# Kernel tuning notes

Hardware: AMD Instinct MI355X
Metric: run time of the kernel (lower is better)

## Reference

```python
import jax, jax.numpy as jnp
import numpy as np

N_NODES = 50000
N_EDGES = 800000


def setup_inputs() -> dict:
    key = jax.random.key(0)
    ks = jax.random.split(key, 8)
    return {
        "x": jax.random.normal(ks[0], (N_NODES, 256), dtype=jnp.float32),
        "adj_vals": jax.random.uniform(ks[1], (N_EDGES,), dtype=jnp.float32),
        "rows": jax.random.randint(ks[2], (N_EDGES,), 0, N_NODES, dtype=jnp.int32),
        "cols": jax.random.randint(ks[3], (N_EDGES,), 0, N_NODES, dtype=jnp.int32),
        "W1": jax.random.normal(ks[4], (256, 256), dtype=jnp.float32) * (1.0 / np.sqrt(256)),
        "b1": jnp.zeros((256,), dtype=jnp.float32),
        "W2": jax.random.normal(ks[5], (256, 256), dtype=jnp.float32) * (1.0 / np.sqrt(256)),
        "b2": jnp.zeros((256,), dtype=jnp.float32),
        "W3": jax.random.normal(ks[6], (256, 128), dtype=jnp.float32) * (1.0 / np.sqrt(256)),
        "b3": jnp.zeros((128,), dtype=jnp.float32),
    }


def reference(x, adj_vals, rows, cols, W1, b1, W2, b2, W3, b3):
    n = x.shape[0]

    def spmm(h):
        # sparse adjacency matmul: out[r] += val * h[c] over all edges (r, c)
        return jax.ops.segment_sum(adj_vals[:, None] * h[cols], rows, num_segments=n)

    # GCNLayer: adj @ (x @ W) + b ; ReLU between layers (dropout p=0 => identity)
    h = jax.nn.relu(spmm(x @ W1) + b1)
    h = jax.nn.relu(spmm(h @ W2) + b2)
    return spmm(h @ W3) + b3
```

## Files before the change

### kernel.cpp

```cpp
#include <hip/hip_runtime.h>
#include <hip/hip_bf16.h>


#define N_NODES 50000
#define N_EDGES 800000
#define KDIM 256
#define BK 32
#define ELLCAP 64
#define ELLB 782
#define TRB 640

typedef __attribute__((ext_vector_type(8))) short short8;
typedef __attribute__((ext_vector_type(4))) float f32x4;

__device__ __forceinline__ ushort f2bf(float f) {
    union { float f; unsigned u; } x; x.f = f;
    unsigned r = x.u + 0x7fffu + ((x.u >> 16) & 1u);
    return (ushort)(r >> 16);
}
__device__ __forceinline__ float bf2f(ushort u) {
    union { unsigned u; float f; } x; x.u = ((unsigned)u) << 16;
    return x.f;
}

__device__ __forceinline__ void gld_lds16(const void* g, void* l) {
    __builtin_amdgcn_global_load_lds(
        (const __attribute__((address_space(1))) void*)g,
        (__attribute__((address_space(3))) void*)l, 16, 0, 0);
}

__global__ __launch_bounds__(256) void transpose_ell_kernel(
        const float* __restrict__ W1, const float* __restrict__ W2,
        const float* __restrict__ W3, ushort* __restrict__ Wt1,
        ushort* __restrict__ Wt2, ushort* __restrict__ Wt3,
        const int* __restrict__ rows, const int* __restrict__ cols,
        const float* __restrict__ vals, int* __restrict__ cnt,
        int2* __restrict__ cv) {
    int b = blockIdx.x;
    if (b < TRB) {
        int id = b * 256 + threadIdx.x;
        if (id < 65536) {
            int n = id >> 8, k = id & 255;
            Wt1[n * 256 + k] = f2bf(W1[k * 256 + n]);
        } else if (id < 131072) {
            int i = id - 65536, n = i >> 8, k = i & 255;
            Wt2[n * 256 + k] = f2bf(W2[k * 256 + n]);
        } else {
            int i = id - 131072, n = i >> 8, k = i & 255;
            Wt3[n * 256 + k] = f2bf(W3[k * 128 + n]);
        }
    } else {
        int e0 = ((b - TRB) * 256 + threadIdx.x) * 4;
        if (e0 < N_EDGES) {
            int4   r4 = *(const int4*)&rows[e0];
            int4   c4 = *(const int4*)&cols[e0];
            float4 v4 = *(const float4*)&vals[e0];
            int p0 = atomicAdd(&cnt[r4.x], 1);
            cv[(r4.x << 6) + p0] = make_int2(c4.x, __float_as_int(v4.x));
            int p1 = atomicAdd(&cnt[r4.y], 1);
            cv[(r4.y << 6) + p1] = make_int2(c4.y, __float_as_int(v4.y));
            int p2 = atomicAdd(&cnt[r4.z], 1);
            cv[(r4.z << 6) + p2] = make_int2(c4.z, __float_as_int(v4.z));
            int p3 = atomicAdd(&cnt[r4.w], 1);
            cv[(r4.w << 6) + p3] = make_int2(c4.w, __float_as_int(v4.w));
        }
    }
}


template <bool AFP32>
__device__ __forceinline__ void gemm_body(
        const void* __restrict__ Ain, const ushort* __restrict__ Wt,
        ushort* __restrict__ C, int M, int N, int bx, int by) {
    __shared__ char smem[AFP32 ? 49152 : 32768];
    const int ABYTES = AFP32 ? 16384 : 8192;

    int t = threadIdx.x;
    int lane = t & 63;
    int w = t >> 6;
    int wbase = w * 64;
    int row0 = bx * 128, col0 = by * 128;
    int wm2 = w & 1, wn2 = w >> 1;
    int wm = wm2 * 64, wn = wn2 * 64;
    int q = lane >> 4, mi = lane & 15;

    char* Ab0 = smem;
    char* Ab1 = smem + ABYTES;
    char* Bb0 = smem + 2 * ABYTES;
    char* Bb1 = smem + 2 * ABYTES + 8192;

    const float*  Af = (const float*)Ain;
    const ushort* Au = (const ushort*)Ain;

    auto stageA = [&](char* dst, int k0) {
        if (AFP32) {
            #pragma unroll
            for (int i = 0; i < 4; i++) {
                int D = i * 256 + t;
                int h = D >> 9, s = D & 511;
                int f = s >> 6, lp = s & 63;
                int row = row0 + (f >> 2) * 64 + (f & 3) * 16 + (lp & 15);
                if (row >= M) row = M - 1;
                const float* g = Af + (size_t)row * KDIM + k0 + (lp >> 4) * 8 + h * 4;
                gld_lds16(g, dst + (i * 256 + wbase) * 16);
            }
        } else {
            #pragma unroll
            for (int i = 0; i < 2; i++) {
                int D = i * 256 + t;
                int f = D >> 6, lp = D & 63;
                int row = row0 + (f >> 2) * 64 + (f & 3) * 16 + (lp & 15);
                if (row >= M) row = M - 1;
                const ushort* g = Au + (size_t)row * KDIM + k0 + (lp >> 4) * 8;
                gld_lds16(g, dst + (i * 256 + wbase) * 16);
            }
        }
    };
    auto stageB = [&](char* dst, int k0) {
        #pragma unroll
        for (int i = 0; i < 2; i++) {
            int D = i * 256 + t;
            int f = D >> 6, lp = D & 63;
            int col = col0 + (f >> 2) * 64 + (f & 3) * 16 + (lp & 15);
            const ushort* g = Wt + (size_t)col * KDIM + k0 + (lp >> 4) * 8;
            gld_lds16(g, dst + (i * 256 + wbase) * 16);
        }
    };

    f32x4 acc[4][4];
    #pragma unroll
    for (int i = 0; i < 4; i++)
        #pragma unroll
        for (int j = 0; j < 4; j++) acc[i][j] = (f32x4)0.f;

    stageA(Ab0, 0);
    stageB(Bb0, 0);
    __syncthreads();

    #pragma unroll
    for (int kt = 0; kt < 8; kt++) {
        char* Acur = (kt & 1) ? Ab1 : Ab0;
        char* Bcur = (kt & 1) ? Bb1 : Bb0;
        if (kt < 7) {
            stageA((kt & 1) ? Ab0 : Ab1, (kt + 1) * BK);
            stageB((kt & 1) ? Bb0 : Bb1, (kt + 1) * BK);
        }

        short8 af[4], bfr[4];
        if (AFP32) {
            const float* As = (const float*)Acur;
            #pragma unroll
            for (int mt = 0; mt < 4; mt++) {
                int gA = (wm2 * 4 + mt) * 64 + lane;
                f32x4 lo = *(const f32x4*)(As + gA * 4);
                f32x4 hi = *(const f32x4*)(As + 2048 + gA * 4);
                af[mt][0] = (short)f2bf(lo[0]); af[mt][1] = (short)f2bf(lo[1]);
                af[mt][2] = (short)f2bf(lo[2]); af[mt][3] = (short)f2bf(lo[3]);
                af[mt][4] = (short)f2bf(hi[0]); af[mt][5] = (short)f2bf(hi[1]);
                af[mt][6] = (short)f2bf(hi[2]); af[mt][7] = (short)f2bf(hi[3]);
            }
        } else {
            #pragma unroll
            for (int mt = 0; mt < 4; mt++)
                af[mt] = *(const short8*)(Acur + ((wm2 * 4 + mt) * 64 + lane) * 16);
        }
        #pragma unroll
        for (int nt = 0; nt < 4; nt++)
            bfr[nt] = *(const short8*)(Bcur + ((wn2 * 4 + nt) * 64 + lane) * 16);

        #pragma unroll
        for (int mt = 0; mt < 4; mt++)
            #pragma unroll
            for (int nt = 0; nt < 4; nt++)
                acc[mt][nt] = __builtin_amdgcn_mfma_f32_16x16x32_bf16(
                    af[mt], bfr[nt], acc[mt][nt], 0, 0, 0);

        __syncthreads();
    }

    ushort* Cs = (ushort*)smem;
    #pragma unroll
    for (int mt = 0; mt < 4; mt++)
        #pragma unroll
        for (int r = 0; r < 4; r++)
            #pragma unroll
            for (int nt = 0; nt < 4; nt++)
                Cs[(wm + mt * 16 + q * 4 + r) * 128 + wn + nt * 16 + mi] =
                    f2bf(acc[mt][nt][r]);
    __syncthreads();
    #pragma unroll
    for (int i = 0; i < 8; i++) {
        int idx = i * 256 + t;
        int rr = idx >> 4, gc = idx & 15;
        int grow = row0 + rr;
        if (grow < M)
            *(short8*)&C[(size_t)grow * N + col0 + gc * 8] =
                *(const short8*)&Cs[rr * 128 + gc * 8];
    }
}

template <bool AFP32>
__global__ __launch_bounds__(256) void gemm_bf16_kernel(
        const void* __restrict__ Ain, const ushort* __restrict__ Wt,
        ushort* __restrict__ C, int M, int N) {
    gemm_body<AFP32>(Ain, Wt, C, M, N, blockIdx.x, blockIdx.y);
}


template <int F, bool RELU, bool OUT_BF16>
__global__ __launch_bounds__(256) void spmm_kernel(
        const ushort* __restrict__ H, const int* __restrict__ cnt,
        const int2* __restrict__ cv, const float* __restrict__ bias,
        void* __restrict__ out, int nrows) {
    constexpr int FL = F / 8;
    constexpr int EP = 64 / FL;
    constexpr int STEP = EP * 8;
    int wave = threadIdx.x >> 6, lane = threadIdx.x & 63;
    int r = blockIdx.x * 4 + wave;
    if (r >= nrows) return;
    int fl = lane % FL, ep = lane / FL;
    const ushort* Hl = H + fl * 8;

    float acc[8];
    #pragma unroll
    for (int j = 0; j < 8; j++) acc[j] = 0.f;

    int start = r << 6;
    int end = start + cnt[r];
    for (int base = start; base < end; base += STEP) {
        int e0 = base + ep * 8;
        int4 ma = *(const int4*)&cv[e0];
        int4 mb = *(const int4*)&cv[e0 + 2];
        int4 mc = *(const int4*)&cv[e0 + 4];
        int4 md = *(const int4*)&cv[e0 + 6];
        int   c[8];
        float v[8];
        c[0] = ma.x; v[0] = __int_as_float(ma.y);
        c[1] = ma.z; v[1] = __int_as_float(ma.w);
        c[2] = mb.x; v[2] = __int_as_float(mb.y);
        c[3] = mb.z; v[3] = __int_as_float(mb.w);
        c[4] = mc.x; v[4] = __int_as_float(mc.y);
        c[5] = mc.z; v[5] = __int_as_float(mc.w);
        c[6] = md.x; v[6] = __int_as_float(md.y);
        c[7] = md.z; v[7] = __int_as_float(md.w);
        #pragma unroll
        for (int u = 0; u < 8; u++) {
            if (e0 + u >= end) { c[u] = 0; v[u] = 0.f; }
        }
        short8 h[8];
        #pragma unroll
        for (int u = 0; u < 8; u++)
            h[u] = *(const short8*)&Hl[(size_t)c[u] * F];
        #pragma unroll
        for (int j = 0; j < 8; j++) {
            #pragma unroll
            for (int u = 0; u < 8; u++)
                acc[j] += v[u] * bf2f((ushort)h[u][j]);
        }
    }

    #pragma unroll
    for (int off = FL; off < 64; off <<= 1)
        #pragma unroll
        for (int j = 0; j < 8; j++) acc[j] += __shfl_down(acc[j], off, 64);

    if (ep == 0) {
        #pragma unroll
        for (int j = 0; j < 8; j++) {
            float o = acc[j] + bias[fl * 8 + j];
            if (RELU) o = fmaxf(o, 0.f);
            acc[j] = o;
        }
        if (OUT_BF16) {
            short8 ob;
            #pragma unroll
            for (int j = 0; j < 8; j++) ob[j] = (short)f2bf(acc[j]);
            *(short8*)((ushort*)out + (size_t)r * F + fl * 8) = ob;
        } else {
            float* of = (float*)out + (size_t)r * F + fl * 8;
            *(float4*)&of[0] = make_float4(acc[0], acc[1], acc[2], acc[3]);
            *(float4*)&of[4] = make_float4(acc[4], acc[5], acc[6], acc[7]);
        }
    }
}


extern "C" void kernel_launch(void* const* d_in, const int* in_sizes, int n_in,
                              void* d_out, int out_size, void* d_ws, size_t ws_size,
                              hipStream_t stream) {
    const float* x    = (const float*)d_in[0];
    const float* av   = (const float*)d_in[1];
    const int*   rows = (const int*)d_in[2];
    const int*   cols = (const int*)d_in[3];
    const float* W1   = (const float*)d_in[4];
    const float* b1   = (const float*)d_in[5];
    const float* W2   = (const float*)d_in[6];
    const float* b2   = (const float*)d_in[7];
    const float* W3   = (const float*)d_in[8];
    const float* b3   = (const float*)d_in[9];
    float* out = (float*)d_out;

    const int N = N_NODES;

    char* p = (char*)d_ws;
    auto carve = [&](size_t bytes) {
        void* q = (void*)p;
        p += (bytes + 255) & ~(size_t)255;
        return q;
    };
    ushort* bufG = (ushort*)carve((size_t)N * 256 * 2);
    ushort* bufH = (ushort*)carve((size_t)N * 256 * 2);
    ushort* Wt1  = (ushort*)carve((size_t)256 * 256 * 2);
    ushort* Wt2  = (ushort*)carve((size_t)256 * 256 * 2);
    ushort* Wt3  = (ushort*)carve((size_t)128 * 256 * 2);
    int*    cnt  = (int*)carve((size_t)N * 4);
    int2*   cv   = (int2*)carve(((size_t)N * ELLCAP + 128) * 8);

    hipMemsetAsync(cnt, 0, (size_t)N * 4, stream);

    transpose_ell_kernel<<<TRB + ELLB, 256, 0, stream>>>(
        W1, W2, W3, Wt1, Wt2, Wt3, rows, cols, av, cnt, cv);

    gemm_bf16_kernel<true><<<dim3(391, 2), 256, 0, stream>>>(x, Wt1, bufG, N, 256);

    int spmm_blocks = (N + 3) / 4;
    spmm_kernel<256, true, true><<<spmm_blocks, 256, 0, stream>>>(bufG, cnt, cv, b1, bufH, N);
    gemm_bf16_kernel<false><<<dim3(391, 2), 256, 0, stream>>>(bufH, Wt2, bufG, N, 256);
    spmm_kernel<256, true, true><<<spmm_blocks, 256, 0, stream>>>(bufG, cnt, cv, b2, bufH, N);
    gemm_bf16_kernel<false><<<dim3(391, 1), 256, 0, stream>>>(bufH, Wt3, bufG, N, 128);
    spmm_kernel<128, false, false><<<spmm_blocks, 256, 0, stream>>>(bufG, cnt, cv, b3, out, N);
}
```

Measured before the change: 362.2 us.

## Pack ELL entries to 32 bits, pre-convert x to bf16, use full-width row GEMM

Each ELL entry now packs a 16-bit column index and an fp16 value into 32 bits, halving edge metadata traffic in the three SpMM passes. A new prep kernel converts x from fp32 to bf16 up front, so the first GEMM reads bf16. The GEMM is restructured so each block owns 64 rows across the full output width, loading each A tile once. Packing the column index into 16 bits only holds because node ids stay below 65536, and fp16 edge values lose precision.

Result: no change. 360.2 us (-0.6%).

```diff
diff --git a/kernel.cpp b/kernel.cpp
--- a/kernel.cpp
+++ b/kernel.cpp
@@ -1,5 +1,5 @@
 #include <hip/hip_runtime.h>
-#include <hip/hip_bf16.h>
+#include <hip/hip_fp16.h>
 
 
 #define N_NODES 50000
@@ -7,7 +7,8 @@
 #define KDIM 256
 #define BK 32
 #define ELLCAP 64
-#define ELLB 782
+#define ELLB 391
+#define XCB 3125
 #define TRB 640
 
 typedef __attribute__((ext_vector_type(8))) short short8;
@@ -29,16 +30,54 @@
         (__attribute__((address_space(3))) void*)l, 16, 0, 0);
 }
 
-__global__ __launch_bounds__(256) void transpose_ell_kernel(
+__global__ __launch_bounds__(256) void prep_kernel(
         const float* __restrict__ W1, const float* __restrict__ W2,
         const float* __restrict__ W3, ushort* __restrict__ Wt1,
         ushort* __restrict__ Wt2, ushort* __restrict__ Wt3,
         const int* __restrict__ rows, const int* __restrict__ cols,
         const float* __restrict__ vals, int* __restrict__ cnt,
-        int2* __restrict__ cv) {
+        unsigned* __restrict__ cvp, const float* __restrict__ x,
+        ushort* __restrict__ bufX) {
     int b = blockIdx.x;
-    if (b < TRB) {
-        int id = b * 256 + threadIdx.x;
+    if (b < ELLB) {
+        int e0 = (b * 256 + threadIdx.x) * 8;
+        if (e0 < N_EDGES) {
+            int4 ra = *(const int4*)&rows[e0];
+            int4 rb = *(const int4*)&rows[e0 + 4];
+            int4 ca = *(const int4*)&cols[e0];
+            int4 cb = *(const int4*)&cols[e0 + 4];
+            float4 va = *(const float4*)&vals[e0];
+            float4 vb = *(const float4*)&vals[e0 + 4];
+            int   r[8] = {ra.x, ra.y, ra.z, ra.w, rb.x, rb.y, rb.z, rb.w};
+            int   c[8] = {ca.x, ca.y, ca.z, ca.w, cb.x, cb.y, cb.z, cb.w};
+            float v[8] = {va.x, va.y, va.z, va.w, vb.x, vb.y, vb.z, vb.w};
+            #pragma unroll
+            for (int u = 0; u < 8; u++) {
+                int p = atomicAdd(&cnt[r[u]], 1);
+                unsigned pk = ((unsigned)c[u] << 16) |
+                              (unsigned)__half_as_ushort(__float2half_rn(v[u]));
+                cvp[(r[u] << 6) + p] = pk;
+            }
+        }
+    } else if (b < ELLB + XCB) {
+        int base = ((b - ELLB) * 256 + threadIdx.x) * 16;
+        float4 f0 = *(const float4*)&x[base];
+        float4 f1 = *(const float4*)&x[base + 4];
+        float4 f2 = *(const float4*)&x[base + 8];
+        float4 f3 = *(const float4*)&x[base + 12];
+        short8 o0, o1;
+        o0[0] = (short)f2bf(f0.x); o0[1] = (short)f2bf(f0.y);
+        o0[2] = (short)f2bf(f0.z); o0[3] = (short)f2bf(f0.w);
+        o0[4] = (short)f2bf(f1.x); o0[5] = (short)f2bf(f1.y);
+        o0[6] = (short)f2bf(f1.z); o0[7] = (short)f2bf(f1.w);
+        o1[0] = (short)f2bf(f2.x); o1[1] = (short)f2bf(f2.y);
+        o1[2] = (short)f2bf(f2.z); o1[3] = (short)f2bf(f2.w);
+        o1[4] = (short)f2bf(f3.x); o1[5] = (short)f2bf(f3.y);
+        o1[6] = (short)f2bf(f3.z); o1[7] = (short)f2bf(f3.w);
+        *(short8*)&bufX[base] = o0;
+        *(short8*)&bufX[base + 8] = o1;
+    } else {
+        int id = (b - ELLB - XCB) * 256 + threadIdx.x;
         if (id < 65536) {
             int n = id >> 8, k = id & 255;
             Wt1[n * 256 + k] = f2bf(W1[k * 256 + n]);
@@ -49,81 +88,42 @@
             int i = id - 131072, n = i >> 8, k = i & 255;
             Wt3[n * 256 + k] = f2bf(W3[k * 128 + n]);
         }
-    } else {
-        int e0 = ((b - TRB) * 256 + threadIdx.x) * 4;
-        if (e0 < N_EDGES) {
-            int4   r4 = *(const int4*)&rows[e0];
-            int4   c4 = *(const int4*)&cols[e0];
-            float4 v4 = *(const float4*)&vals[e0];
-            int p0 = atomicAdd(&cnt[r4.x], 1);
-            cv[(r4.x << 6) + p0] = make_int2(c4.x, __float_as_int(v4.x));
-            int p1 = atomicAdd(&cnt[r4.y], 1);
-            cv[(r4.y << 6) + p1] = make_int2(c4.y, __float_as_int(v4.y));
-            int p2 = atomicAdd(&cnt[r4.z], 1);
-            cv[(r4.z << 6) + p2] = make_int2(c4.z, __float_as_int(v4.z));
-            int p3 = atomicAdd(&cnt[r4.w], 1);
-            cv[(r4.w << 6) + p3] = make_int2(c4.w, __float_as_int(v4.w));
-        }
-    }
-}
-
-
-template <bool AFP32>
-__device__ __forceinline__ void gemm_body(
-        const void* __restrict__ Ain, const ushort* __restrict__ Wt,
-        ushort* __restrict__ C, int M, int N, int bx, int by) {
-    __shared__ char smem[AFP32 ? 49152 : 32768];
-    const int ABYTES = AFP32 ? 16384 : 8192;
+    }
+}
+
+
+template <int N>
+__global__ __launch_bounds__(N, 4) void gemm_rows_kernel(
+        const ushort* __restrict__ A, const ushort* __restrict__ Wt,
+        ushort* __restrict__ C, int M) {
+    __shared__ char smem[8192 + 2 * N * 64];
 
     int t = threadIdx.x;
     int lane = t & 63;
     int w = t >> 6;
-    int wbase = w * 64;
-    int row0 = bx * 128, col0 = by * 128;
-    int wm2 = w & 1, wn2 = w >> 1;
-    int wm = wm2 * 64, wn = wn2 * 64;
+    int row0 = blockIdx.x * 64;
+    int wn = w * 64;
     int q = lane >> 4, mi = lane & 15;
 
-    char* Ab0 = smem;
-    char* Ab1 = smem + ABYTES;
-    char* Bb0 = smem + 2 * ABYTES;
-    char* Bb1 = smem + 2 * ABYTES + 8192;
-
-    const float*  Af = (const float*)Ain;
-    const ushort* Au = (const ushort*)Ain;
-
-    auto stageA = [&](char* dst, int k0) {
-        if (AFP32) {
-            #pragma unroll
-            for (int i = 0; i < 4; i++) {
-                int D = i * 256 + t;
-                int h = D >> 9, s = D & 511;
-                int f = s >> 6, lp = s & 63;
-                int row = row0 + (f >> 2) * 64 + (f & 3) * 16 + (lp & 15);
-                if (row >= M) row = M - 1;
-                const float* g = Af + (size_t)row * KDIM + k0 + (lp >> 4) * 8 + h * 4;
-                gld_lds16(g, dst + (i * 256 + wbase) * 16);
-            }
-        } else {
-            #pragma unroll
-            for (int i = 0; i < 2; i++) {
-                int D = i * 256 + t;
-                int f = D >> 6, lp = D & 63;
-                int row = row0 + (f >> 2) * 64 + (f & 3) * 16 + (lp & 15);
-                if (row >= M) row = M - 1;
-                const ushort* g = Au + (size_t)row * KDIM + k0 + (lp >> 4) * 8;
-                gld_lds16(g, dst + (i * 256 + wbase) * 16);
-            }
+    auto stageA = [&](int bi, int k0) {
+        char* dst = smem + bi * 4096;
+        #pragma unroll
+        for (int i = 0; i < 256 / N; i++) {
+            int g = i * N + t;
+            int row = row0 + ((g >> 6) << 4) + (g & 15);
+            if (row >= M) row = M - 1;
+            const ushort* src = A + (size_t)row * KDIM + k0 + (((g & 63) >> 4) << 3);
+            gld_lds16(src, dst + (i * N + w * 64) * 16);
         }
     };
-    auto stageB = [&](char* dst, int k0) {
-        #pragma unroll
-        for (int i = 0; i < 2; i++) {
-            int D = i * 256 + t;
-            int f = D >> 6, lp = D & 63;
-            int col = col0 + (f >> 2) * 64 + (f & 3) * 16 + (lp & 15);
-            const ushort* g = Wt + (size_t)col * KDIM + k0 + (lp >> 4) * 8;
-            gld_lds16(g, dst + (i * 256 + wbase) * 16);
+    auto stageB = [&](int bi, int k0) {
+        char* dst = smem + 8192 + bi * (N * 64);
+        #pragma unroll
+        for (int i = 0; i < 4; i++) {
+            int g = i * N + t;
+            int col = ((g >> 6) << 4) + (g & 15);
+            const ushort* src = Wt + (size_t)col * KDIM + k0 + (((g & 63) >> 4) << 3);
+            gld_lds16(src, dst + (i * N + w * 64) * 16);
         }
     };
 
@@ -133,40 +133,27 @@
         #pragma unroll
         for (int j = 0; j < 4; j++) acc[i][j] = (f32x4)0.f;
 
-    stageA(Ab0, 0);
-    stageB(Bb0, 0);
+    stageA(0, 0);
+    stageB(0, 0);
     __syncthreads();
 
     #pragma unroll
     for (int kt = 0; kt < 8; kt++) {
-        char* Acur = (kt & 1) ? Ab1 : Ab0;
-        char* Bcur = (kt & 1) ? Bb1 : Bb0;
+        int cur = kt & 1;
         if (kt < 7) {
-            stageA((kt & 1) ? Ab0 : Ab1, (kt + 1) * BK);
-            stageB((kt & 1) ? Bb0 : Bb1, (kt + 1) * BK);
-        }
+            stageA(cur ^ 1, (kt + 1) * BK);
+            stageB(cur ^ 1, (kt + 1) * BK);
+        }
+        char* Ac = smem + cur * 4096;
+        char* Bc = smem + 8192 + cur * (N * 64);
 
         short8 af[4], bfr[4];
-        if (AFP32) {
-            const float* As = (const float*)Acur;
-            #pragma unroll
-            for (int mt = 0; mt < 4; mt++) {
-                int gA = (wm2 * 4 + mt) * 64 + lane;
-                f32x4 lo = *(const f32x4*)(As + gA * 4);
-                f32x4 hi = *(const f32x4*)(As + 2048 + gA * 4);
-                af[mt][0] = (short)f2bf(lo[0]); af[mt][1] = (short)f2bf(lo[1]);
-                af[mt][2] = (short)f2bf(lo[2]); af[mt][3] = (short)f2bf(lo[3]);
-                af[mt][4] = (short)f2bf(hi[0]); af[mt][5] = (short)f2bf(hi[1]);
-                af[mt][6] = (short)f2bf(hi[2]); af[mt][7] = (short)f2bf(hi[3]);
-            }
-        } else {
-            #pragma unroll
-            for (int mt = 0; mt < 4; mt++)
-                af[mt] = *(const short8*)(Acur + ((wm2 * 4 + mt) * 64 + lane) * 16);
-        }
+        #pragma unroll
+        for (int mt = 0; mt < 4; mt++)
+            af[mt] = *(const short8*)(Ac + (mt * 64 + lane) * 16);
         #pragma unroll
         for (int nt = 0; nt < 4; nt++)
-            bfr[nt] = *(const short8*)(Bcur + ((wn2 * 4 + nt) * 64 + lane) * 16);
+            bfr[nt] = *(const short8*)(Bc + ((w * 4 + nt) * 64 + lane) * 16);
 
         #pragma unroll
         for (int mt = 0; mt < 4; mt++)
@@ -185,32 +172,26 @@
         for (int r = 0; r < 4; r++)
             #pragma unroll
             for (int nt = 0; nt < 4; nt++)
-                Cs[(wm + mt * 16 + q * 4 + r) * 128 + wn + nt * 16 + mi] =
+                Cs[(mt * 16 + q * 4 + r) * N + wn + nt * 16 + mi] =
                     f2bf(acc[mt][nt][r]);
     __syncthreads();
+    constexpr int C8 = N / 8;
     #pragma unroll
     for (int i = 0; i < 8; i++) {
-        int idx = i * 256 + t;
-        int rr = idx >> 4, gc = idx & 15;
+        int idx = i * N + t;
+        int rr = idx / C8, gc = idx % C8;
         int grow = row0 + rr;
         if (grow < M)
-            *(short8*)&C[(size_t)grow * N + col0 + gc * 8] =
-                *(const short8*)&Cs[rr * 128 + gc * 8];
-    }
-}
-
-template <bool AFP32>
-__global__ __launch_bounds__(256) void gemm_bf16_kernel(
-        const void* __restrict__ Ain, const ushort* __restrict__ Wt,
-        ushort* __restrict__ C, int M, int N) {
-    gemm_body<AFP32>(Ain, Wt, C, M, N, blockIdx.x, blockIdx.y);
+            *(short8*)&C[(size_t)grow * N + gc * 8] =
+                *(const short8*)&Cs[rr * N + gc * 8];
+    }
 }
 
 
 template <int F, bool RELU, bool OUT_BF16>
 __global__ __launch_bounds__(256) void spmm_kernel(
         const ushort* __restrict__ H, const int* __restrict__ cnt,
-        const int2* __restrict__ cv, const float* __restrict__ bias,
+        const unsigned* __restrict__ cvp, const float* __restrict__ bias,
         void* __restrict__ out, int nrows) {
     constexpr int FL = F / 8;
     constexpr int EP = 64 / FL;
@@ -229,23 +210,16 @@
     int end = start + cnt[r];
     for (int base = start; base < end; base += STEP) {
         int e0 = base + ep * 8;
-        int4 ma = *(const int4*)&cv[e0];
-        int4 mb = *(const int4*)&cv[e0 + 2];
-        int4 mc = *(const int4*)&cv[e0 + 4];
-        int4 md = *(const int4*)&cv[e0 + 6];
+        uint4 ma = *(const uint4*)&cvp[e0];
+        uint4 mb = *(const uint4*)&cvp[e0 + 4];
+        unsigned mw[8] = {ma.x, ma.y, ma.z, ma.w, mb.x, mb.y, mb.z, mb.w};
         int   c[8];
         float v[8];
-        c[0] = ma.x; v[0] = __int_as_float(ma.y);
-        c[1] = ma.z; v[1] = __int_as_float(ma.w);
-        c[2] = mb.x; v[2] = __int_as_float(mb.y);
-        c[3] = mb.z; v[3] = __int_as_float(mb.w);
-        c[4] = mc.x; v[4] = __int_as_float(mc.y);
-        c[5] = mc.z; v[5] = __int_as_float(mc.w);
-        c[6] = md.x; v[6] = __int_as_float(md.y);
-        c[7] = md.z; v[7] = __int_as_float(md.w);
         #pragma unroll
         for (int u = 0; u < 8; u++) {
-            if (e0 + u >= end) { c[u] = 0; v[u] = 0.f; }
+            bool ok = (e0 + u < end);
+            c[u] = ok ? (int)(mw[u] >> 16) : 0;
+            v[u] = ok ? __half2float(__ushort_as_half((ushort)mw[u])) : 0.f;
         }
         short8 h[8];
         #pragma unroll
@@ -308,25 +282,24 @@
         p += (bytes + 255) & ~(size_t)255;
         return q;
     };
-    ushort* bufG = (ushort*)carve((size_t)N * 256 * 2);
-    ushort* bufH = (ushort*)carve((size_t)N * 256 * 2);
-    ushort* Wt1  = (ushort*)carve((size_t)256 * 256 * 2);
-    ushort* Wt2  = (ushort*)carve((size_t)256 * 256 * 2);
-    ushort* Wt3  = (ushort*)carve((size_t)128 * 256 * 2);
-    int*    cnt  = (int*)carve((size_t)N * 4);
-    int2*   cv   = (int2*)carve(((size_t)N * ELLCAP + 128) * 8);
+    ushort*   bufG = (ushort*)carve((size_t)N * 256 * 2);
+    ushort*   bufH = (ushort*)carve((size_t)N * 256 * 2);
+    ushort*   Wt1  = (ushort*)carve((size_t)256 * 256 * 2);
+    ushort*   Wt2  = (ushort*)carve((size_t)256 * 256 * 2);
+    ushort*   Wt3  = (ushort*)carve((size_t)128 * 256 * 2);
+    int*      cnt  = (int*)carve((size_t)N * 4);
+    unsigned* cvp  = (unsigned*)carve(((size_t)N * ELLCAP + 128) * 4);
 
     hipMemsetAsync(cnt, 0, (size_t)N * 4, stream);
 
-    transpose_ell_kernel<<<TRB + ELLB, 256, 0, stream>>>(
-        W1, W2, W3, Wt1, Wt2, Wt3, rows, cols, av, cnt, cv);
-
-    gemm_bf16_kernel<true><<<dim3(391, 2), 256, 0, stream>>>(x, Wt1, bufG, N, 256);
+    prep_kernel<<<ELLB + XCB + TRB, 256, 0, stream>>>(
+        W1, W2, W3, Wt1, Wt2, Wt3, rows, cols, av, cnt, cvp, x, bufH);
 
     int spmm_blocks = (N + 3) / 4;
-    spmm_kernel<256, true, true><<<spmm_blocks, 256, 0, stream>>>(bufG, cnt, cv, b1, bufH, N);
-    gemm_bf16_kernel<false><<<dim3(391, 2), 256, 0, stream>>>(bufH, Wt2, bufG, N, 256);
-    spmm_kernel<256, true, true><<<spmm_blocks, 256, 0, stream>>>(bufG, cnt, cv, b2, bufH, N);
-    gemm_bf16_kernel<false><<<dim3(391, 1), 256, 0, stream>>>(bufH, Wt3, bufG, N, 128);
-    spmm_kernel<128, false, false><<<spmm_blocks, 256, 0, stream>>>(bufG, cnt, cv, b3, out, N);
-}
+    gemm_rows_kernel<256><<<782, 256, 0, stream>>>(bufH, Wt1, bufG, N);
+    spmm_kernel<256, true, true><<<spmm_blocks, 256, 0, stream>>>(bufG, cnt, cvp, b1, bufH, N);
+    gemm_rows_kernel<256><<<782, 256, 0, stream>>>(bufH, Wt2, bufG, N);
+    spmm_kernel<256, true, true><<<spmm_blocks, 256, 0, stream>>>(bufG, cnt, cvp, b2, bufH, N);
+    gemm_rows_kernel<128><<<782, 128, 0, stream>>>(bufH, Wt3, bufG, N);
+    spmm_kernel<128, false, false><<<spmm_blocks, 256, 0, stream>>>(bufG, cnt, cvp, b3, out, N);
+}
```
